# Performance work log

Measured on AMD Instinct MI355X. Metric: run time of the kernel, lower is better.

The kernel has to match this reference:

```python
import jax, jax.numpy as jnp
import numpy as np

B, S, H = 4, 4096, 2048
CIN, COUT, K, G = 4096, 4096, 4, 8


def setup_inputs() -> dict:
    key = jax.random.key(0)
    ks = jax.random.split(key, 7)
    sc = 0.02
    return {
        "x": jax.random.normal(ks[0], (B, S, H), dtype=jnp.float32),
        "W_in": jax.random.normal(ks[1], (CIN, H), dtype=jnp.float32) * sc,
        "b_in": jax.random.normal(ks[2], (CIN,), dtype=jnp.float32) * sc,
        "conv_w": jax.random.normal(ks[3], (COUT, CIN // G, K), dtype=jnp.float32) * sc,
        "conv_b": jax.random.normal(ks[4], (COUT,), dtype=jnp.float32) * sc,
        "W_out": jax.random.normal(ks[5], (H, COUT), dtype=jnp.float32) * sc,
        "b_out": jax.random.normal(ks[6], (H,), dtype=jnp.float32) * sc,
    }


def reference(x, W_in, b_in, conv_w, conv_b, W_out, b_out):
    # input projection: [B,S,H] -> [B,S,CIN]
    h = jnp.einsum("bsh,ch->bsc", x, W_in) + b_in
    # causal grouped conv1d over sequence dim: NCW layout
    h = h.transpose(0, 2, 1)  # [B, CIN, S]
    k = conv_w.shape[2]
    groups = h.shape[1] // conv_w.shape[1]
    y = jax.lax.conv_general_dilated(
        h, conv_w,
        window_strides=(1,),
        padding=[(k - 1, 0)],  # left-pad only == pad k-1 then trim trailing
        feature_group_count=groups,
        dimension_numbers=("NCH", "OIH", "NCH"),
    )  # [B, COUT, S]
    y = jax.nn.silu(y + conv_b[None, :, None])
    y = y.transpose(0, 2, 1)  # [B, S, COUT]
    # output projection: [B,S,COUT] -> [B,S,H]
    out = jnp.einsum("bsc,hc->bsh", y, W_out) + b_out
    return out
```

## Files before the change

### kernel.cpp

```cpp
#include <hip/hip_runtime.h>
#include <cstdint>
#include <cstddef>

static constexpr int Bn   = 4;
static constexpr int Sn   = 4096;
static constexpr int Hn   = 2048;
static constexpr int CINn = 4096;
static constexpr int COUTn= 4096;
static constexpr int GCn  = 512;
static constexpr int Kt   = 4;
static constexpr int Mn   = Bn * Sn;
static constexpr int SPn  = Sn + 3;

typedef _Float16 half8 __attribute__((ext_vector_type(8)));
typedef _Float16 half4 __attribute__((ext_vector_type(4)));
typedef float    floatx4 __attribute__((ext_vector_type(4)));


__global__ void cvt_f32_f16(const float* __restrict__ src, _Float16* __restrict__ dst, int n4) {
    int i = blockIdx.x * blockDim.x + threadIdx.x;
    if (i < n4) {
        float4 v = ((const float4*)src)[i];
        half4 h;
        h[0] = (_Float16)v.x; h[1] = (_Float16)v.y;
        h[2] = (_Float16)v.z; h[3] = (_Float16)v.w;
        ((half4*)dst)[i] = h;
    }
}

__global__ void cvt_convw(const float* __restrict__ src, _Float16* __restrict__ dst) {
    int t = blockIdx.x * blockDim.x + threadIdx.x;
    int co = t >> 9, ci = t & 511;
    float4 v = ((const float4*)src)[(co << 9) + ci];
    size_t base = (size_t)co * 2048 + ci;
    dst[base]        = (_Float16)v.x;
    dst[base + 512]  = (_Float16)v.y;
    dst[base + 1024] = (_Float16)v.z;
    dst[base + 1536] = (_Float16)v.w;
}

__global__ void zero_pads(_Float16* __restrict__ Hp) {
    int t = blockIdx.x * blockDim.x + threadIdx.x;
    int b = t / (3 * CINn);
    int off = t - b * (3 * CINn);
    Hp[(size_t)b * SPn * CINn + off] = (_Float16)0.f;
}


__device__ __forceinline__ void async16(const void* g, void* l) {
    __builtin_amdgcn_global_load_lds(
        (__attribute__((address_space(1))) void*)(g),
        (__attribute__((address_space(3))) void*)(l),
        16, 0, 0);
}

#define BAR()  __builtin_amdgcn_s_barrier()
#define SB0()  __builtin_amdgcn_sched_barrier(0)
#define WL0()  asm volatile("s_waitcnt lgkmcnt(0)" ::: "memory")
#define WV(n)  asm volatile("s_waitcnt vmcnt(" #n ")" ::: "memory")

template <int MODE>
__global__ __launch_bounds__(512, 2) void gemm8(
    const _Float16* __restrict__ A,
    const _Float16* __restrict__ Bw,
    const float* __restrict__ bias,
    void* __restrict__ outp,
    int Kd, int Ntiles)
{
    __shared__ __align__(16) _Float16 smem[2][2][256 * 64];

    const int t  = threadIdx.x;
    const int w  = t >> 6;
    const int l  = t & 63;
    const int wm = w >> 2;
    const int wn = w & 3;

    const int nwg = (int)gridDim.x;
    const int bid = (int)blockIdx.x;
    const int swz = (bid & 7) * (nwg >> 3) + (bid >> 3);
    const int mt = swz / Ntiles, nt = swz - mt * Ntiles;
    const int m0 = mt * 256, n0 = nt * 256;

    const int sr  = t >> 3;
    const int scb = ((t & 7) ^ (sr & 7)) << 3;
    const _Float16* pa[4];
    const _Float16* pb[4];
    #pragma unroll
    for (int q = 0; q < 4; ++q) {
        int ma = m0 + q * 64 + sr;
        if (MODE == 1) {
            pa[q] = A + ((size_t)((ma >> 12) * SPn + (ma & 4095)) << 12) + (n0 >> 9) * 512 + scb;
        } else {
            pa[q] = A + (size_t)ma * Kd + scb;
        }
        pb[q] = Bw + (size_t)(n0 + q * 64 + sr) * Kd + scb;
    }
    const int wst = w * 512;

    const int fr = l & 15, quad = l >> 4, sw = fr & 7;

    floatx4 acc[8][4] = {};
    half8 af[4][2];
    half8 bf[4][2];

    const int NT = Kd >> 6;

#define KADJ(kk) ((MODE == 1) ? ((kk) + (((kk) >> 9) * 3584)) : (kk))
#define STA(b, q, ko) async16(pa[q] + (ko), &smem[b][0][(q) * 4096 + wst])
#define STB(b, q, ko) async16(pb[q] + (ko), &smem[b][1][(q) * 4096 + wst])

#define READ_A(cb, mh) do { \
    _Pragma("unroll") for (int mf = 0; mf < 4; ++mf) \
    _Pragma("unroll") for (int ks = 0; ks < 2; ++ks) { \
        int row = wm * 128 + (mh) * 64 + mf * 16 + fr; \
        af[mf][ks] = *(const half8*)(&smem[cb][0][row * 64 + ((((ks << 2) + quad) ^ sw) << 3)]); \
    } } while (0)

#define READ_B(cb, nh) do { \
    _Pragma("unroll") for (int nf = 0; nf < 2; ++nf) \
    _Pragma("unroll") for (int ks = 0; ks < 2; ++ks) { \
        int row = wn * 64 + ((nh) * 2 + nf) * 16 + fr; \
        bf[(nh) * 2 + nf][ks] = *(const half8*)(&smem[cb][1][row * 64 + ((((ks << 2) + quad) ^ sw) << 3)]); \
    } } while (0)

#define MMA(mh, nh) do { \
    _Pragma("unroll") for (int mf = 0; mf < 4; ++mf) \
    _Pragma("unroll") for (int nf = 0; nf < 2; ++nf) \
    _Pragma("unroll") for (int ks = 0; ks < 2; ++ks) \
        acc[(mh) * 4 + mf][(nh) * 2 + nf] = __builtin_amdgcn_mfma_f32_16x16x32_f16( \
            af[mf][ks], bf[(nh) * 2 + nf][ks], acc[(mh) * 4 + mf][(nh) * 2 + nf], 0, 0, 0); \
    } while (0)

    {
        STA(0, 0, 0); STA(0, 1, 0); STA(0, 2, 0); STA(0, 3, 0);
        STB(0, 0, 0); STB(0, 1, 0); STB(0, 2, 0); STB(0, 3, 0);
        const int ka1 = KADJ(64);
        STA(1, 0, ka1); STA(1, 2, ka1);
        STB(1, 0, 64); STB(1, 1, 64); STB(1, 2, 64); STB(1, 3, 64);
        WV(6);
        BAR();
    }

    for (int tt = 0; tt < NT; ++tt) {
        const int cur = tt & 1, nxt = cur ^ 1;
        const bool s1 = (tt + 1 < NT), s2 = (tt + 2 < NT);
        const int ka1 = KADJ((tt + 1) << 6);
        const int ka2 = KADJ((tt + 2) << 6);
        const int kb2 = (tt + 2) << 6;

        READ_A(cur, 0);
        READ_B(cur, 0);
        if (s1) { STA(nxt, 1, ka1); STA(nxt, 3, ka1); }
        SB0(); BAR();
        WL0(); SB0();
        __builtin_amdgcn_s_setprio(1);
        MMA(0, 0);
        __builtin_amdgcn_s_setprio(0);
        SB0(); BAR();

        READ_B(cur, 1);
        if (s2) { STA(cur, 0, ka2); STA(cur, 2, ka2); }
        SB0(); BAR();
        WL0(); SB0();
        __builtin_amdgcn_s_setprio(1);
        MMA(0, 1);
        __builtin_amdgcn_s_setprio(0);
        SB0();
        if (s2) { WV(8); } else { WV(0); }
        SB0(); BAR();

        READ_A(cur, 1);
        if (s2) { STB(cur, 0, kb2); STB(cur, 1, kb2); }
        SB0(); BAR();
        WL0(); SB0();
        __builtin_amdgcn_s_setprio(1);
        MMA(1, 0);
        __builtin_amdgcn_s_setprio(0);
        SB0(); BAR();

        if (s2) { STB(cur, 2, kb2); STB(cur, 3, kb2); }
        SB0(); BAR();
        WL0(); SB0();
        __builtin_amdgcn_s_setprio(1);
        MMA(1, 1);
        __builtin_amdgcn_s_setprio(0);
        SB0();
        if (s2) { WV(8); } else { WV(0); }
        SB0(); BAR();
    }

    #pragma unroll
    for (int nf = 0; nf < 4; ++nf) {
        const int ncol = n0 + wn * 64 + nf * 16 + fr;
        const float bv = bias[ncol];
        #pragma unroll
        for (int mf = 0; mf < 8; ++mf) {
            const int mb = m0 + wm * 128 + mf * 16 + quad * 4;
            #pragma unroll
            for (int r = 0; r < 4; ++r) {
                const int m = mb + r;
                float v = acc[mf][nf][r] + bv;
                if (MODE == 0) {
                    const size_t row = (size_t)((m >> 12) * SPn + 3 + (m & 4095));
                    ((_Float16*)outp)[(row << 12) + ncol] = (_Float16)v;
                } else if (MODE == 1) {
                    v = v * (1.0f / (1.0f + __expf(-v)));
                    ((_Float16*)outp)[((size_t)m << 12) + ncol] = (_Float16)v;
                } else {
                    ((float*)outp)[((size_t)m << 11) + ncol] = v;
                }
            }
        }
    }
#undef KADJ
#undef STA
#undef STB
#undef READ_A
#undef READ_B
#undef MMA
}


extern "C" void kernel_launch(void* const* d_in, const int* in_sizes, int n_in,
                              void* d_out, int out_size, void* d_ws, size_t ws_size,
                              hipStream_t stream) {
    const float* x      = (const float*)d_in[0];
    const float* W_in   = (const float*)d_in[1];
    const float* b_in   = (const float*)d_in[2];
    const float* conv_w = (const float*)d_in[3];
    const float* conv_b = (const float*)d_in[4];
    const float* W_out  = (const float*)d_in[5];
    const float* b_out  = (const float*)d_in[6];
    float* out = (float*)d_out;

    char* ws = (char*)d_ws;
    _Float16* Xh  = (_Float16*)(ws);
    _Float16* W1h = (_Float16*)(ws + 67108864);
    _Float16* Wch = (_Float16*)(ws + 83886080);
    _Float16* W2h = (_Float16*)(ws + 100663296);
    _Float16* Hp  = (_Float16*)(ws + 117440512);
    _Float16* Yh  = (_Float16*)(ws + 251756544);
    (void)ws_size; (void)in_sizes; (void)n_in; (void)out_size;

    cvt_f32_f16<<<32768, 256, 0, stream>>>(x,     Xh,  Mn * Hn / 4);
    cvt_f32_f16<<<8192,  256, 0, stream>>>(W_in,  W1h, CINn * Hn / 4);
    cvt_convw <<<8192,  256, 0, stream>>>(conv_w, Wch);
    cvt_f32_f16<<<8192,  256, 0, stream>>>(W_out, W2h, Hn * COUTn / 4);
    zero_pads <<<192,   256, 0, stream>>>(Hp);

    gemm8<0><<<(Mn / 256) * (CINn / 256), 512, 0, stream>>>(Xh, W1h, b_in, (void*)Hp, Hn, CINn / 256);
    gemm8<1><<<(Mn / 256) * (COUTn / 256), 512, 0, stream>>>(Hp, Wch, conv_b, (void*)Yh, GCn * Kt, COUTn / 256);
    gemm8<2><<<(Mn / 256) * (Hn / 256), 512, 0, stream>>>(Yh, W2h, b_out, (void*)out, COUTn, Hn / 256);
}
```

Before: 1.086 ms.

## Restructure GEMM main loop to prefetch next tile's LDS fragments during MMAs

Rewrites the inner k-loop schedule of the shared GEMM kernel. LDS fragment reads for the next k-tile now overlap the current tile's MFMA phases, using separate A-fragment register sets and a different async global-to-LDS issue order. This cuts barriers per iteration from eight to two and replaces per-row pointer arrays with a base pointer plus stride. It also raises wave priority across the whole loop. The cost is more live registers, which could cause spilling under the 2-block launch bound, and a subtle risk of LDS read/write races.

Result: faster. 1.049 ms (-3.3%).

```diff
diff --git a/kernel.cpp b/kernel.cpp
--- a/kernel.cpp
+++ b/kernel.cpp
@@ -58,6 +58,8 @@
 #define SB0()  __builtin_amdgcn_sched_barrier(0)
 #define WL0()  asm volatile("s_waitcnt lgkmcnt(0)" ::: "memory")
 #define WV(n)  asm volatile("s_waitcnt vmcnt(" #n ")" ::: "memory")
+#define PRIO1() __builtin_amdgcn_s_setprio(1)
+#define PRIO0() __builtin_amdgcn_s_setprio(0)
 
 template <int MODE>
 __global__ __launch_bounds__(512, 2) void gemm8(
@@ -83,111 +85,113 @@
 
     const int sr  = t >> 3;
     const int scb = ((t & 7) ^ (sr & 7)) << 3;
-    const _Float16* pa[4];
-    const _Float16* pb[4];
-    #pragma unroll
-    for (int q = 0; q < 4; ++q) {
-        int ma = m0 + q * 64 + sr;
-        if (MODE == 1) {
-            pa[q] = A + ((size_t)((ma >> 12) * SPn + (ma & 4095)) << 12) + (n0 >> 9) * 512 + scb;
-        } else {
-            pa[q] = A + (size_t)ma * Kd + scb;
-        }
-        pb[q] = Bw + (size_t)(n0 + q * 64 + sr) * Kd + scb;
-    }
+    const _Float16* pa0;
+    if (MODE == 1) {
+        const int ma = m0 + sr;
+        pa0 = A + ((size_t)((ma >> 12) * SPn + (ma & 4095)) << 12) + (n0 >> 9) * 512 + scb;
+    } else {
+        pa0 = A + (size_t)(m0 + sr) * Kd + scb;
+    }
+    const _Float16* pb0 = Bw + (size_t)(n0 + sr) * Kd + scb;
+    const size_t aq = (MODE == 1) ? (size_t)(64 * 4096) : (size_t)64 * Kd;
+    const size_t bq = (size_t)64 * Kd;
     const int wst = w * 512;
 
     const int fr = l & 15, quad = l >> 4, sw = fr & 7;
 
     floatx4 acc[8][4] = {};
-    half8 af[4][2];
+    half8 afA[4][2];
+    half8 afB[4][2];
     half8 bf[4][2];
 
     const int NT = Kd >> 6;
 
 #define KADJ(kk) ((MODE == 1) ? ((kk) + (((kk) >> 9) * 3584)) : (kk))
-#define STA(b, q, ko) async16(pa[q] + (ko), &smem[b][0][(q) * 4096 + wst])
-#define STB(b, q, ko) async16(pb[q] + (ko), &smem[b][1][(q) * 4096 + wst])
-
-#define READ_A(cb, mh) do { \
+#define STA(b, q, ko) async16(pa0 + (size_t)(q) * aq + (ko), &smem[b][0][(q) * 4096 + wst])
+#define STB(b, q, ko) async16(pb0 + (size_t)(q) * bq + (ko), &smem[b][1][(q) * 4096 + wst])
+
+#define LCOL(ks) ((((ks << 2) + quad) ^ sw) << 3)
+
+#define RD_B0(cb) do { \
+    _Pragma("unroll") for (int nf = 0; nf < 2; ++nf) \
+    _Pragma("unroll") for (int ks = 0; ks < 2; ++ks) { \
+        int row = wn * 64 + nf * 16 + fr; \
+        bf[nf][ks] = *(const half8*)(&smem[cb][1][row * 64 + LCOL(ks)]); \
+    } } while (0)
+
+#define RD_B1(cb) do { \
+    _Pragma("unroll") for (int nf = 0; nf < 2; ++nf) \
+    _Pragma("unroll") for (int ks = 0; ks < 2; ++ks) { \
+        int row = wn * 64 + 32 + nf * 16 + fr; \
+        bf[2 + nf][ks] = *(const half8*)(&smem[cb][1][row * 64 + LCOL(ks)]); \
+    } } while (0)
+
+#define RD_A1(cb) do { \
     _Pragma("unroll") for (int mf = 0; mf < 4; ++mf) \
     _Pragma("unroll") for (int ks = 0; ks < 2; ++ks) { \
-        int row = wm * 128 + (mh) * 64 + mf * 16 + fr; \
-        af[mf][ks] = *(const half8*)(&smem[cb][0][row * 64 + ((((ks << 2) + quad) ^ sw) << 3)]); \
-    } } while (0)
-
-#define READ_B(cb, nh) do { \
-    _Pragma("unroll") for (int nf = 0; nf < 2; ++nf) \
-    _Pragma("unroll") for (int ks = 0; ks < 2; ++ks) { \
-        int row = wn * 64 + ((nh) * 2 + nf) * 16 + fr; \
-        bf[(nh) * 2 + nf][ks] = *(const half8*)(&smem[cb][1][row * 64 + ((((ks << 2) + quad) ^ sw) << 3)]); \
-    } } while (0)
-
-#define MMA(mh, nh) do { \
+        int row = wm * 128 + 64 + mf * 16 + fr; \
+        afB[mf][ks] = *(const half8*)(&smem[cb][0][row * 64 + LCOL(ks)]); \
+    } } while (0)
+
+#define RD_A0_LO(cb) do { \
+    _Pragma("unroll") for (int mf = 0; mf < 2; ++mf) \
+    _Pragma("unroll") for (int ks = 0; ks < 2; ++ks) { \
+        int row = wm * 128 + mf * 16 + fr; \
+        afA[mf][ks] = *(const half8*)(&smem[cb][0][row * 64 + LCOL(ks)]); \
+    } } while (0)
+
+#define RD_A0_HI(cb) do { \
+    _Pragma("unroll") for (int mf = 2; mf < 4; ++mf) \
+    _Pragma("unroll") for (int ks = 0; ks < 2; ++ks) { \
+        int row = wm * 128 + mf * 16 + fr; \
+        afA[mf][ks] = *(const half8*)(&smem[cb][0][row * 64 + LCOL(ks)]); \
+    } } while (0)
+
+#define MMA_PH(AF, mh, nh) do { \
     _Pragma("unroll") for (int mf = 0; mf < 4; ++mf) \
     _Pragma("unroll") for (int nf = 0; nf < 2; ++nf) \
     _Pragma("unroll") for (int ks = 0; ks < 2; ++ks) \
         acc[(mh) * 4 + mf][(nh) * 2 + nf] = __builtin_amdgcn_mfma_f32_16x16x32_f16( \
-            af[mf][ks], bf[(nh) * 2 + nf][ks], acc[(mh) * 4 + mf][(nh) * 2 + nf], 0, 0, 0); \
+            AF[mf][ks], bf[(nh) * 2 + nf][ks], acc[(mh) * 4 + mf][(nh) * 2 + nf], 0, 0, 0); \
     } while (0)
 
     {
         STA(0, 0, 0); STA(0, 1, 0); STA(0, 2, 0); STA(0, 3, 0);
         STB(0, 0, 0); STB(0, 1, 0); STB(0, 2, 0); STB(0, 3, 0);
         const int ka1 = KADJ(64);
-        STA(1, 0, ka1); STA(1, 2, ka1);
+        STA(1, 0, ka1); STA(1, 1, ka1); STA(1, 2, ka1); STA(1, 3, ka1);
         STB(1, 0, 64); STB(1, 1, 64); STB(1, 2, 64); STB(1, 3, 64);
-        WV(6);
-        BAR();
-    }
-
+        WV(0); BAR(); SB0();
+        RD_A0_LO(0); RD_A0_HI(0); RD_B0(0);
+    }
+
+    PRIO1();
     for (int tt = 0; tt < NT; ++tt) {
         const int cur = tt & 1, nxt = cur ^ 1;
         const bool s1 = (tt + 1 < NT), s2 = (tt + 2 < NT);
-        const int ka1 = KADJ((tt + 1) << 6);
         const int ka2 = KADJ((tt + 2) << 6);
         const int kb2 = (tt + 2) << 6;
 
-        READ_A(cur, 0);
-        READ_B(cur, 0);
-        if (s1) { STA(nxt, 1, ka1); STA(nxt, 3, ka1); }
-        SB0(); BAR();
-        WL0(); SB0();
-        __builtin_amdgcn_s_setprio(1);
-        MMA(0, 0);
-        __builtin_amdgcn_s_setprio(0);
-        SB0(); BAR();
-
-        READ_B(cur, 1);
-        if (s2) { STA(cur, 0, ka2); STA(cur, 2, ka2); }
-        SB0(); BAR();
-        WL0(); SB0();
-        __builtin_amdgcn_s_setprio(1);
-        MMA(0, 1);
-        __builtin_amdgcn_s_setprio(0);
-        SB0();
-        if (s2) { WV(8); } else { WV(0); }
-        SB0(); BAR();
-
-        READ_A(cur, 1);
-        if (s2) { STB(cur, 0, kb2); STB(cur, 1, kb2); }
-        SB0(); BAR();
-        WL0(); SB0();
-        __builtin_amdgcn_s_setprio(1);
-        MMA(1, 0);
-        __builtin_amdgcn_s_setprio(0);
-        SB0(); BAR();
-
-        if (s2) { STB(cur, 2, kb2); STB(cur, 3, kb2); }
-        SB0(); BAR();
-        WL0(); SB0();
-        __builtin_amdgcn_s_setprio(1);
-        MMA(1, 1);
-        __builtin_amdgcn_s_setprio(0);
-        SB0();
-        if (s2) { WV(8); } else { WV(0); }
-        SB0(); BAR();
-    }
+        RD_B1(cur);
+        MMA_PH(afA, 0, 0);
+        PRIO0(); WL0(); BAR(); SB0(); PRIO1();
+        if (s2) { STA(cur, 0, ka2); STA(cur, 2, ka2);
+                  STB(cur, 0, kb2); STB(cur, 1, kb2); STB(cur, 2, kb2); STB(cur, 3, kb2); }
+
+        RD_A1(cur);
+        MMA_PH(afA, 0, 1);
+        PRIO0();
+        if (s2) { WV(6); } else { WV(0); }
+        WL0(); BAR(); SB0(); PRIO1();
+        if (s2) { STA(cur, 1, ka2); STA(cur, 3, ka2); }
+
+        if (s1) RD_A0_LO(nxt);
+        MMA_PH(afB, 1, 0);
+
+        if (s1) { RD_A0_HI(nxt); RD_B0(nxt); }
+        MMA_PH(afB, 1, 1);
+    }
+    PRIO0();
 
     #pragma unroll
     for (int nf = 0; nf < 4; ++nf) {
@@ -215,9 +219,13 @@
 #undef KADJ
 #undef STA
 #undef STB
-#undef READ_A
-#undef READ_B
-#undef MMA
+#undef LCOL
+#undef RD_B0
+#undef RD_B1
+#undef RD_A1
+#undef RD_A0_LO
+#undef RD_A0_HI
+#undef MMA_PH
 }
 
 
```
